# Kernel tuning notes

Measured on AMD Instinct MI355X. Metric: run time of the kernel, lower is better.

## Reference

```python
import jax, jax.numpy as jnp
import numpy as np

N_ATOM = 2048
C_ATOM = 128
C_PAIR = 16
N_HEADS = 4
BLOCK = 128
EPS = 1e-5


def _layernorm(x):
    mu = jnp.mean(x, axis=-1, keepdims=True)
    var = jnp.mean(jnp.square(x - mu), axis=-1, keepdims=True)
    return (x - mu) / jnp.sqrt(var + EPS)


def setup_inputs() -> dict:
    key = jax.random.key(0)
    ks = jax.random.split(key, 12)
    s = 0.02
    x = jax.random.normal(ks[0], (N_ATOM, C_ATOM), jnp.float32)
    pair_emb = jax.random.normal(ks[1], (N_ATOM, N_ATOM, C_PAIR), jnp.float32)
    block_index = jax.random.randint(ks[2], (N_ATOM, BLOCK), 0, N_ATOM, jnp.int64)
    Wq = jax.random.normal(ks[3], (C_ATOM, C_ATOM), jnp.float32) * s
    Wk = jax.random.normal(ks[4], (C_ATOM, C_ATOM), jnp.float32) * s
    Wv = jax.random.normal(ks[5], (C_ATOM, C_ATOM), jnp.float32) * s
    Wb = jax.random.normal(ks[6], (N_HEADS, 1), jnp.float32) * s  # nn.Linear(1, num_heads)
    Wout = jax.random.normal(ks[7], (C_ATOM, C_ATOM), jnp.float32) * s
    W1 = jax.random.normal(ks[8], (4 * C_ATOM, C_ATOM), jnp.float32) * s
    b1 = jnp.zeros((4 * C_ATOM,), jnp.float32)
    W2 = jax.random.normal(ks[9], (C_ATOM, 4 * C_ATOM), jnp.float32) * s
    b2 = jnp.zeros((C_ATOM,), jnp.float32)
    return {"x": x, "pair_emb": pair_emb, "block_index": block_index,
            "Wq": Wq, "Wk": Wk, "Wv": Wv, "Wb": Wb, "Wout": Wout,
            "W1": W1, "b1": b1, "W2": W2, "b2": b2}


def reference(x, pair_emb, block_index, Wq, Wk, Wv, Wb, Wout, W1, b1, W2, b2):
    N = x.shape[0]
    d_head = C_ATOM // N_HEADS
    h = _layernorm(x)
    q = (h @ Wq.T).reshape(N, N_HEADS, d_head)
    k = (h @ Wk.T).reshape(N, N_HEADS, d_head)
    v = (h @ Wv.T).reshape(N, N_HEADS, d_head)

    # pair bias per head: mean over c_pair, then Linear(1 -> n_heads)
    pair_mean = jnp.mean(pair_emb, axis=-1)              # [N, N]
    pair_bias = pair_mean[..., None] * Wb[:, 0]          # [N, N, H]

    # local block-sparse attention: each query i attends to keys block_index[i]
    k_g = k[block_index]                                 # [N, B, H, d]
    v_g = v[block_index]                                 # [N, B, H, d]
    rows = jnp.arange(N)[:, None]
    bias = pair_bias[rows, block_index]                  # [N, B, H]

    scale = 1.0 / jnp.sqrt(jnp.asarray(d_head, q.dtype))
    scores = jnp.einsum('nhd,nbhd->nhb', q, k_g) * scale + jnp.transpose(bias, (0, 2, 1))
    attn = jax.nn.softmax(scores, axis=-1)               # [N, H, B]
    attn_out = jnp.einsum('nhb,nbhd->nhd', attn, v_g).reshape(N, C_ATOM)

    x = x + attn_out @ Wout.T
    h2 = _layernorm(x)
    mlp = jax.nn.silu(h2 @ W1.T + b1) @ W2.T + b2
    return x + mlp
```

## Files before the change

kernel.cpp:

```cpp
#include <hip/hip_runtime.h>
#include <hip/hip_bf16.h>

#define N_ATOMS 2048
#define C_DIM   128
#define C_PAIR  16
#define BLK_K   128
#define LN_EPS  1e-5f

typedef float f32x4 __attribute__((ext_vector_type(4)));
typedef short s16x8 __attribute__((ext_vector_type(8)));

__device__ __forceinline__ float bf_lo(unsigned int p) {
    union { unsigned int i; float f; } u; u.i = p << 16; return u.f;
}
__device__ __forceinline__ float bf_hi(unsigned int p) {
    union { unsigned int i; float f; } u; u.i = p & 0xffff0000u; return u.f;
}
__device__ __forceinline__ float bf2f(unsigned short s) {
    union { unsigned int i; float f; } u; u.i = ((unsigned int)s) << 16; return u.f;
}
__device__ __forceinline__ unsigned short f2bf(float f) {
    union { float f; unsigned int i; } u; u.f = f;
    const unsigned int r = u.i + 0x7fffu + ((u.i >> 16) & 1u);
    return (unsigned short)(r >> 16);
}

__device__ __forceinline__ s16x8 lda_frag(const unsigned short* base,
                                          int rowBytes, int kstep, int lane) {
    const int m    = lane & 15;
    const int koff = kstep * 64 + ((lane >> 4) << 4);
    const int addr = m * rowBytes + (koff ^ ((m & 7) << 4));
    return *reinterpret_cast<const s16x8*>(
        reinterpret_cast<const char*>(base) + addr);
}

__device__ void pack_unit(int u, int lane,
                          const float* __restrict__ Wout,
                          const float* __restrict__ W1,
                          const float* __restrict__ W2,
                          unsigned short* __restrict__ WoutP,
                          unsigned short* __restrict__ W1P,
                          unsigned short* __restrict__ W2P)
{
    const float* W; unsigned short* P; int K, local;
    if (u < 32)       { W = Wout; P = WoutP; K = 128; local = u; }
    else if (u < 160) { W = W1;   P = W1P;   K = 128; local = u - 32; }
    else              { W = W2;   P = W2P;   K = 512; local = u - 160; }
    const int ksteps = K >> 5;
    const int ntile  = local / ksteps;
    const int kstep  = local - ntile * ksteps;
    const int n  = ntile * 16 + (lane & 15);
    const int k0 = kstep * 32 + ((lane >> 4) << 3);
    const float4* src = reinterpret_cast<const float4*>(W + (size_t)n * K + k0);
    const float4 a = src[0], b = src[1];
    s16x8 o;
    o[0] = (short)f2bf(a.x); o[1] = (short)f2bf(a.y);
    o[2] = (short)f2bf(a.z); o[3] = (short)f2bf(a.w);
    o[4] = (short)f2bf(b.x); o[5] = (short)f2bf(b.y);
    o[6] = (short)f2bf(b.z); o[7] = (short)f2bf(b.w);
    reinterpret_cast<s16x8*>(P)[local * 64 + lane] = o;
}

__global__ __launch_bounds__(768) void ln_qkv_kernel(
    const float* __restrict__ x,
    const float* __restrict__ Wq, const float* __restrict__ Wk,
    const float* __restrict__ Wv,
    const float* __restrict__ Wout, const float* __restrict__ W1,
    const float* __restrict__ W2,
    float* __restrict__ q,
    unsigned short* __restrict__ kb, unsigned short* __restrict__ vb,
    unsigned short* __restrict__ WoutP, unsigned short* __restrict__ W1P,
    unsigned short* __restrict__ W2P)
{
    __shared__ __align__(16) float hs[8][128];
    __shared__ __align__(16) float part[2][3][8][128];
    const int t = threadIdx.x;
    const int bid = blockIdx.x;
    const int row0 = bid * 8;

    if (t < 64) pack_unit(bid, t, Wout, W1, W2, WoutP, W1P, W2P);
    else if (bid < 32 && t >= 64 && t < 128)
        pack_unit(256 + bid, t - 64, Wout, W1, W2, WoutP, W1P, W2P);

    if (t < 256) {
        const int r = t >> 5, l = t & 31;
        const float4 xv = reinterpret_cast<const float4*>(
            x + (size_t)(row0 + r) * C_DIM)[l];
        float s  = xv.x + xv.y + xv.z + xv.w;
        float ss = xv.x*xv.x + xv.y*xv.y + xv.z*xv.z + xv.w*xv.w;
        #pragma unroll
        for (int m = 16; m >= 1; m >>= 1) {
            s  += __shfl_xor(s,  m);
            ss += __shfl_xor(ss, m);
        }
        const float mu  = s * (1.0f / 128.0f);
        const float var = ss * (1.0f / 128.0f) - mu * mu;
        const float inv = rsqrtf(var + LN_EPS);
        float4 hv;
        hv.x = (xv.x - mu) * inv;
        hv.y = (xv.y - mu) * inv;
        hv.z = (xv.z - mu) * inv;
        hv.w = (xv.w - mu) * inv;
        *reinterpret_cast<float4*>(&hs[r][l * 4]) = hv;
    }
    __syncthreads();

    {
        const int p  = t >> 8;
        const int u  = t & 255;
        const int c  = u & 127;
        const int kh = u >> 7;
        const float* Wp = (p == 0) ? Wq : (p == 1) ? Wk : Wv;
        const float4* W4 = reinterpret_cast<const float4*>(
            Wp + (size_t)c * C_DIM + kh * 64);
        float acc[8] = {0.f,0.f,0.f,0.f,0.f,0.f,0.f,0.f};
        #pragma unroll
        for (int jq = 0; jq < 16; ++jq) {
            const float4 w4 = W4[jq];
            #pragma unroll
            for (int r = 0; r < 8; ++r) {
                const float4 h4 = *reinterpret_cast<const float4*>(
                    &hs[r][kh * 64 + jq * 4]);
                acc[r] += w4.x*h4.x + w4.y*h4.y + w4.z*h4.z + w4.w*h4.w;
            }
        }
        #pragma unroll
        for (int r = 0; r < 8; ++r) part[kh][p][r][c] = acc[r];
    }
    __syncthreads();

    {
        const int p  = t >> 8;
        const int u  = t & 255;
        const int c  = u & 127;
        const int rh = u >> 7;
        #pragma unroll
        for (int rr = 0; rr < 4; ++rr) {
            const int r = rh * 4 + rr;
            const float val = part[0][p][r][c] + part[1][p][r][c];
            const size_t off = (size_t)(row0 + r) * C_DIM + c;
            if (p == 0)      q[off]  = val;
            else if (p == 1) kb[off] = f2bf(val);
            else             vb[off] = f2bf(val);
        }
    }
}

__global__ __launch_bounds__(1024) void attn_mlp_kernel(
    const float* __restrict__ q, const unsigned short* __restrict__ kb,
    const unsigned short* __restrict__ vb, const float* __restrict__ pair,
    const int*  __restrict__ bidx, const float* __restrict__ Wb,
    const float* __restrict__ x,
    const unsigned short* __restrict__ WoutP,
    const unsigned short* __restrict__ W1P, const float* __restrict__ b1,
    const unsigned short* __restrict__ W2P, const float* __restrict__ b2,
    float* __restrict__ out)
{
    __shared__ __align__(16) float qS[8][128];
    __shared__ __align__(16) int   idxS[8][128];
    __shared__ __align__(16) float S[8][4][128];
    __shared__ __align__(16) float ys[8][128];
    __shared__ __align__(16) unsigned short aoB[16][128];
    __shared__ __align__(16) unsigned short h2B[16][128];
    __shared__ __align__(16) unsigned short gsB[16][512];

    const int t = threadIdx.x;
    const int row0 = blockIdx.x * 8;
    const int r = t >> 7;
    const int u = t & 127;
    const int row = row0 + r;
    const int wv = t >> 6, lane = t & 63;

    const int j = bidx[(size_t)row * BLK_K + u];
    idxS[r][u] = j;
    qS[r][u] = q[(size_t)row * C_DIM + u];
    if (t < 256) {
        const int r2 = t >> 5, l = t & 31;
        const float4 xv = reinterpret_cast<const float4*>(
            x + (size_t)(row0 + r2) * C_DIM)[l];
        *reinterpret_cast<float4*>(&ys[r2][l * 4]) = xv;
    } else if (t < 384) {
        const uint4 z = {0,0,0,0};
        reinterpret_cast<uint4*>(&aoB[8][0])[t - 256] = z;
    } else if (t < 512) {
        const uint4 z = {0,0,0,0};
        reinterpret_cast<uint4*>(&h2B[8][0])[t - 384] = z;
    } else {
        const uint4 z = {0,0,0,0};
        reinterpret_cast<uint4*>(&gsB[8][0])[t - 512] = z;
    }
    const f32x4* pr = reinterpret_cast<const f32x4*>(
        pair + ((size_t)row * N_ATOMS + (size_t)j) * C_PAIR);
    const f32x4 p0 = __builtin_nontemporal_load(pr + 0);
    const f32x4 p1 = __builtin_nontemporal_load(pr + 1);
    const f32x4 p2 = __builtin_nontemporal_load(pr + 2);
    const f32x4 p3 = __builtin_nontemporal_load(pr + 3);
    __syncthreads();

    {
        const uint4* kr = reinterpret_cast<const uint4*>(kb + (size_t)j * C_DIM);
        const float4* q4 = reinterpret_cast<const float4*>(&qS[r][0]);
        float sc[4];
        #pragma unroll
        for (int h = 0; h < 4; ++h) {
            float a = 0.f;
            #pragma unroll
            for (int d = 0; d < 4; ++d) {
                const uint4  kk = kr[h * 4 + d];
                const float4 qa = q4[h * 8 + d * 2];
                const float4 qc = q4[h * 8 + d * 2 + 1];
                a += bf_lo(kk.x)*qa.x + bf_hi(kk.x)*qa.y
                   + bf_lo(kk.y)*qa.z + bf_hi(kk.y)*qa.w;
                a += bf_lo(kk.z)*qc.x + bf_hi(kk.z)*qc.y
                   + bf_lo(kk.w)*qc.z + bf_hi(kk.w)*qc.w;
            }
            sc[h] = a;
        }
        const float pm = (p0.x+p0.y+p0.z+p0.w + p1.x+p1.y+p1.z+p1.w +
                          p2.x+p2.y+p2.z+p2.w + p3.x+p3.y+p3.z+p3.w) * (1.0f/16.0f);
        const float scale = 0.17677669529663687f;
        #pragma unroll
        for (int h = 0; h < 4; ++h)
            S[r][h][u] = sc[h] * scale + pm * Wb[h];
    }
    __syncthreads();

    {
        const int g = u >> 5, l = u & 31;
        const float v0 = S[r][g][l],      v1 = S[r][g][l + 32],
                    v2 = S[r][g][l + 64], v3 = S[r][g][l + 96];
        float mx = fmaxf(fmaxf(v0, v1), fmaxf(v2, v3));
        #pragma unroll
        for (int m = 16; m >= 1; m >>= 1) mx = fmaxf(mx, __shfl_xor(mx, m));
        const float e0 = __expf(v0 - mx), e1 = __expf(v1 - mx),
                    e2 = __expf(v2 - mx), e3 = __expf(v3 - mx);
        float sm = e0 + e1 + e2 + e3;
        #pragma unroll
        for (int m = 16; m >= 1; m >>= 1) sm += __shfl_xor(sm, m);
        const float rs = 1.0f / sm;
        S[r][g][l]      = e0 * rs;
        S[r][g][l + 32] = e1 * rs;
        S[r][g][l + 64] = e2 * rs;
        S[r][g][l + 96] = e3 * rs;
    }
    __syncthreads();

    {
        const int hh = u >> 5;
        const float4* Sv = reinterpret_cast<const float4*>(&S[r][hh][0]);
        const int4*   iv = reinterpret_cast<const int4*>(&idxS[r][0]);
        float acc = 0.f;
        #pragma unroll 8
        for (int bq = 0; bq < 32; ++bq) {
            const float4 s4 = Sv[bq];
            const int4   j4 = iv[bq];
            acc += s4.x * bf2f(vb[(size_t)j4.x * C_DIM + u]);
            acc += s4.y * bf2f(vb[(size_t)j4.y * C_DIM + u]);
            acc += s4.z * bf2f(vb[(size_t)j4.z * C_DIM + u]);
            acc += s4.w * bf2f(vb[(size_t)j4.w * C_DIM + u]);
        }
        *reinterpret_cast<unsigned short*>(
            reinterpret_cast<char*>(&aoB[0][0]) +
            r * 256 + (((u * 2)) ^ ((r & 7) << 4))) = f2bf(acc);
    }
    __syncthreads();

    if (wv < 8) {
        f32x4 acc = {0.f, 0.f, 0.f, 0.f};
        const s16x8* Bp = reinterpret_cast<const s16x8*>(WoutP);
        #pragma unroll
        for (int ks = 0; ks < 4; ++ks) {
            const s16x8 a = lda_frag(&aoB[0][0], 256, ks, lane);
            const s16x8 b = Bp[(wv * 4 + ks) * 64 + lane];
            acc = __builtin_amdgcn_mfma_f32_16x16x32_bf16(a, b, acc, 0, 0, 0);
        }
        if (lane < 32) {
            const int c = wv * 16 + (lane & 15);
            #pragma unroll
            for (int i = 0; i < 4; ++i) {
                const int m = ((lane >> 4) << 2) + i;
                ys[m][c] += acc[i];
            }
        }
    }
    __syncthreads();

    if (t < 256) {
        const int rr = t >> 5, l = t & 31;
        const float4 yv = *reinterpret_cast<const float4*>(&ys[rr][l * 4]);
        float s  = yv.x + yv.y + yv.z + yv.w;
        float ss = yv.x*yv.x + yv.y*yv.y + yv.z*yv.z + yv.w*yv.w;
        #pragma unroll
        for (int m = 16; m >= 1; m >>= 1) {
            s  += __shfl_xor(s,  m);
            ss += __shfl_xor(ss, m);
        }
        const float mu  = s * (1.0f / 128.0f);
        const float var = ss * (1.0f / 128.0f) - mu * mu;
        const float inv = rsqrtf(var + LN_EPS);
        union { unsigned long long u64; unsigned short u16[4]; } pk;
        pk.u16[0] = f2bf((yv.x - mu) * inv);
        pk.u16[1] = f2bf((yv.y - mu) * inv);
        pk.u16[2] = f2bf((yv.z - mu) * inv);
        pk.u16[3] = f2bf((yv.w - mu) * inv);
        *reinterpret_cast<unsigned long long*>(
            reinterpret_cast<char*>(&h2B[0][0]) +
            rr * 256 + ((l * 8) ^ ((rr & 7) << 4))) = pk.u64;
    }
    __syncthreads();

    {
        s16x8 afr[4];
        #pragma unroll
        for (int ks = 0; ks < 4; ++ks) afr[ks] = lda_frag(&h2B[0][0], 256, ks, lane);
        const s16x8* Bp = reinterpret_cast<const s16x8*>(W1P);
        #pragma unroll
        for (int tt = 0; tt < 2; ++tt) {
            const int tile = wv * 2 + tt;
            f32x4 acc = {0.f, 0.f, 0.f, 0.f};
            #pragma unroll
            for (int ks = 0; ks < 4; ++ks) {
                const s16x8 b = Bp[(tile * 4 + ks) * 64 + lane];
                acc = __builtin_amdgcn_mfma_f32_16x16x32_bf16(afr[ks], b, acc, 0, 0, 0);
            }
            if (lane < 32) {
                const int c = tile * 16 + (lane & 15);
                const float bb = b1[c];
                #pragma unroll
                for (int i = 0; i < 4; ++i) {
                    const int m = ((lane >> 4) << 2) + i;
                    const float g = acc[i] + bb;
                    const float sv = g / (1.0f + __expf(-g));
                    *reinterpret_cast<unsigned short*>(
                        reinterpret_cast<char*>(&gsB[0][0]) +
                        m * 1024 + ((c * 2) ^ ((m & 7) << 4))) = f2bf(sv);
                }
            }
        }
    }
    __syncthreads();

    if (wv < 8) {
        f32x4 acc = {0.f, 0.f, 0.f, 0.f};
        const s16x8* Bp = reinterpret_cast<const s16x8*>(W2P);
        #pragma unroll
        for (int ks = 0; ks < 16; ++ks) {
            const s16x8 a = lda_frag(&gsB[0][0], 1024, ks, lane);
            const s16x8 b = Bp[(wv * 16 + ks) * 64 + lane];
            acc = __builtin_amdgcn_mfma_f32_16x16x32_bf16(a, b, acc, 0, 0, 0);
        }
        if (lane < 32) {
            const int c = wv * 16 + (lane & 15);
            const float bb = b2[c];
            #pragma unroll
            for (int i = 0; i < 4; ++i) {
                const int m = ((lane >> 4) << 2) + i;
                out[(size_t)(row0 + m) * C_DIM + c] = ys[m][c] + bb + acc[i];
            }
        }
    }
}

extern "C" void kernel_launch(void* const* d_in, const int* in_sizes, int n_in,
                              void* d_out, int out_size, void* d_ws, size_t ws_size,
                              hipStream_t stream)
{
    const float* x    = (const float*)d_in[0];
    const float* pair = (const float*)d_in[1];
    const int*   bidx = (const int*)  d_in[2];
    const float* Wq   = (const float*)d_in[3];
    const float* Wk   = (const float*)d_in[4];
    const float* Wv   = (const float*)d_in[5];
    const float* Wb   = (const float*)d_in[6];
    const float* Wout = (const float*)d_in[7];
    const float* W1   = (const float*)d_in[8];
    const float* b1   = (const float*)d_in[9];
    const float* W2   = (const float*)d_in[10];
    const float* b2   = (const float*)d_in[11];
    float* out = (float*)d_out;

    char* ws = (char*)d_ws;
    float*          q     = (float*)ws;
    unsigned short* kb    = (unsigned short*)(ws + (1 << 20));
    unsigned short* vb    = (unsigned short*)(ws + (1 << 20) + (1 << 19));
    unsigned short* WoutP = (unsigned short*)(ws + (2 << 20));
    unsigned short* W1P   = (unsigned short*)(ws + (2 << 20) + (32 << 10));
    unsigned short* W2P   = (unsigned short*)(ws + (2 << 20) + (160 << 10));

    hipLaunchKernelGGL(ln_qkv_kernel, dim3(N_ATOMS / 8), dim3(768), 0, stream,
                       x, Wq, Wk, Wv, Wout, W1, W2, q, kb, vb, WoutP, W1P, W2P);
    hipLaunchKernelGGL(attn_mlp_kernel, dim3(N_ATOMS / 8), dim3(1024), 0, stream,
                       q, kb, vb, pair, bidx, Wb, x, WoutP, W1P, b1, W2P, b2, out);
}
```

Measured before the change: 43.57 us.

## Compute LN+QKV projection with bf16 MFMA over 16-row tiles

Replaces the scalar fp32 QKV projection, which used split-K partial sums in shared memory, with bf16 MFMA 16x16x32. Layernormed rows go into a swizzled bf16 shared tile, and each wave converts its weight fragments from global fp32 on the fly. Blocks now cover 16 rows with 512 threads, halving the grid, and the weight-packing work is redistributed to match. q is now computed from bf16 inputs, which lowers its precision, and every block re-reads and re-converts the fp32 weights.

```diff
diff --git a/kernel.cpp b/kernel.cpp
--- a/kernel.cpp
+++ b/kernel.cpp
@@ -61,7 +61,7 @@
     reinterpret_cast<s16x8*>(P)[local * 64 + lane] = o;
 }
 
-__global__ __launch_bounds__(768) void ln_qkv_kernel(
+__global__ __launch_bounds__(512) void ln_qkv_kernel(
     const float* __restrict__ x,
     const float* __restrict__ Wq, const float* __restrict__ Wk,
     const float* __restrict__ Wv,
@@ -72,17 +72,17 @@
     unsigned short* __restrict__ WoutP, unsigned short* __restrict__ W1P,
     unsigned short* __restrict__ W2P)
 {
-    __shared__ __align__(16) float hs[8][128];
-    __shared__ __align__(16) float part[2][3][8][128];
+    __shared__ __align__(16) unsigned short hB[16][128];
     const int t = threadIdx.x;
     const int bid = blockIdx.x;
-    const int row0 = bid * 8;
-
-    if (t < 64) pack_unit(bid, t, Wout, W1, W2, WoutP, W1P, W2P);
-    else if (bid < 32 && t >= 64 && t < 128)
-        pack_unit(256 + bid, t - 64, Wout, W1, W2, WoutP, W1P, W2P);
-
-    if (t < 256) {
+    const int row0 = bid * 16;
+
+    if (t < 64)       pack_unit(bid * 2,     t,       Wout, W1, W2, WoutP, W1P, W2P);
+    else if (t < 128) pack_unit(bid * 2 + 1, t - 64,  Wout, W1, W2, WoutP, W1P, W2P);
+    else if (t < 192 && bid < 32)
+                      pack_unit(256 + bid,   t - 128, Wout, W1, W2, WoutP, W1P, W2P);
+
+    {
         const int r = t >> 5, l = t & 31;
         const float4 xv = reinterpret_cast<const float4*>(
             x + (size_t)(row0 + r) * C_DIM)[l];
@@ -96,52 +96,49 @@
         const float mu  = s * (1.0f / 128.0f);
         const float var = ss * (1.0f / 128.0f) - mu * mu;
         const float inv = rsqrtf(var + LN_EPS);
-        float4 hv;
-        hv.x = (xv.x - mu) * inv;
-        hv.y = (xv.y - mu) * inv;
-        hv.z = (xv.z - mu) * inv;
-        hv.w = (xv.w - mu) * inv;
-        *reinterpret_cast<float4*>(&hs[r][l * 4]) = hv;
-    }
-    __syncthreads();
-
-    {
-        const int p  = t >> 8;
-        const int u  = t & 255;
-        const int c  = u & 127;
-        const int kh = u >> 7;
-        const float* Wp = (p == 0) ? Wq : (p == 1) ? Wk : Wv;
-        const float4* W4 = reinterpret_cast<const float4*>(
-            Wp + (size_t)c * C_DIM + kh * 64);
-        float acc[8] = {0.f,0.f,0.f,0.f,0.f,0.f,0.f,0.f};
-        #pragma unroll
-        for (int jq = 0; jq < 16; ++jq) {
-            const float4 w4 = W4[jq];
-            #pragma unroll
-            for (int r = 0; r < 8; ++r) {
-                const float4 h4 = *reinterpret_cast<const float4*>(
-                    &hs[r][kh * 64 + jq * 4]);
-                acc[r] += w4.x*h4.x + w4.y*h4.y + w4.z*h4.z + w4.w*h4.w;
-            }
-        }
-        #pragma unroll
-        for (int r = 0; r < 8; ++r) part[kh][p][r][c] = acc[r];
-    }
-    __syncthreads();
-
-    {
-        const int p  = t >> 8;
-        const int u  = t & 255;
-        const int c  = u & 127;
-        const int rh = u >> 7;
-        #pragma unroll
-        for (int rr = 0; rr < 4; ++rr) {
-            const int r = rh * 4 + rr;
-            const float val = part[0][p][r][c] + part[1][p][r][c];
-            const size_t off = (size_t)(row0 + r) * C_DIM + c;
-            if (p == 0)      q[off]  = val;
-            else if (p == 1) kb[off] = f2bf(val);
-            else             vb[off] = f2bf(val);
+        union { unsigned long long u64; unsigned short u16[4]; } pk;
+        pk.u16[0] = f2bf((xv.x - mu) * inv);
+        pk.u16[1] = f2bf((xv.y - mu) * inv);
+        pk.u16[2] = f2bf((xv.z - mu) * inv);
+        pk.u16[3] = f2bf((xv.w - mu) * inv);
+        *reinterpret_cast<unsigned long long*>(
+            reinterpret_cast<char*>(&hB[0][0]) +
+            r * 256 + ((l * 8) ^ ((r & 7) << 4))) = pk.u64;
+    }
+    __syncthreads();
+
+    {
+        const int wv = t >> 6, lane = t & 63;
+        s16x8 afr[4];
+        #pragma unroll
+        for (int ks = 0; ks < 4; ++ks) afr[ks] = lda_frag(&hB[0][0], 256, ks, lane);
+
+        const int n = wv * 16 + (lane & 15);
+        #pragma unroll
+        for (int p = 0; p < 3; ++p) {
+            const float* W = (p == 0) ? Wq : (p == 1) ? Wk : Wv;
+            f32x4 acc = {0.f, 0.f, 0.f, 0.f};
+            #pragma unroll
+            for (int ks = 0; ks < 4; ++ks) {
+                const int k0 = ks * 32 + ((lane >> 4) << 3);
+                const float4* src = reinterpret_cast<const float4*>(
+                    W + (size_t)n * C_DIM + k0);
+                const float4 a = src[0], b = src[1];
+                s16x8 bfr;
+                bfr[0] = (short)f2bf(a.x); bfr[1] = (short)f2bf(a.y);
+                bfr[2] = (short)f2bf(a.z); bfr[3] = (short)f2bf(a.w);
+                bfr[4] = (short)f2bf(b.x); bfr[5] = (short)f2bf(b.y);
+                bfr[6] = (short)f2bf(b.z); bfr[7] = (short)f2bf(b.w);
+                acc = __builtin_amdgcn_mfma_f32_16x16x32_bf16(afr[ks], bfr, acc, 0, 0, 0);
+            }
+            #pragma unroll
+            for (int ii = 0; ii < 4; ++ii) {
+                const int m = ((lane >> 4) << 2) + ii;
+                const size_t off = (size_t)(row0 + m) * C_DIM + n;
+                if (p == 0)      q[off]  = acc[ii];
+                else if (p == 1) kb[off] = f2bf(acc[ii]);
+                else             vb[off] = f2bf(acc[ii]);
+            }
         }
     }
 }
@@ -387,7 +384,7 @@
     unsigned short* W1P   = (unsigned short*)(ws + (2 << 20) + (32 << 10));
     unsigned short* W2P   = (unsigned short*)(ws + (2 << 20) + (160 << 10));
 
-    hipLaunchKernelGGL(ln_qkv_kernel, dim3(N_ATOMS / 8), dim3(768), 0, stream,
+    hipLaunchKernelGGL(ln_qkv_kernel, dim3(N_ATOMS / 16), dim3(512), 0, stream,
                        x, Wq, Wk, Wv, Wout, W1, W2, q, kb, vb, WoutP, W1P, W2P);
     hipLaunchKernelGGL(attn_mlp_kernel, dim3(N_ATOMS / 8), dim3(1024), 0, stream,
                        q, kb, vb, pair, bidx, Wb, x, WoutP, W1P, b1, W2P, b2, out);
```

Measured after the change: 42.76 us. Within noise of the previous version (-1.9%).
